# Kernel optimization log

Hardware: AMD Instinct MI355X
Metric: run time of the kernel (lower is better)

Reference implementation:

```python
import jax, jax.numpy as jnp
import numpy as np
from jax import lax

EMBED = 512
HEADS = 8
KD = EMBED // HEADS  # key_dim == head_dim (value_factor=1)


def setup_inputs() -> dict:
    key = jax.random.key(0)
    ks = jax.random.split(key, 13)
    b, h, w = 4, 128, 128
    s = 0.02
    return {
        "x": jax.random.normal(ks[0], (b, h, w, EMBED), jnp.float32),
        "mask_h": jax.random.normal(ks[1], (HEADS, h, h), jnp.float32),
        "mask_w": jax.random.normal(ks[2], (HEADS, w, w), jnp.float32),
        "Wq": jax.random.normal(ks[3], (EMBED, EMBED), jnp.float32) * s,
        "bq": jnp.zeros((EMBED,), jnp.float32),
        "Wk": jax.random.normal(ks[4], (EMBED, EMBED), jnp.float32) * s,
        "bk": jnp.zeros((EMBED,), jnp.float32),
        "Wv": jax.random.normal(ks[5], (EMBED, EMBED), jnp.float32) * s,
        "bv": jnp.zeros((EMBED,), jnp.float32),
        "lepe_w": jax.random.normal(ks[6], (5, 5, 1, EMBED), jnp.float32) * s,  # depthwise 5x5, HWIO
        "lepe_b": jnp.zeros((EMBED,), jnp.float32),
        "Wo": jax.random.normal(ks[7], (EMBED, EMBED), jnp.float32) * s,
        "bo": jnp.zeros((EMBED,), jnp.float32),
    }


def reference(x, mask_h, mask_w, Wq, bq, Wk, bk, Wv, bv, lepe_w, lepe_b, Wo, bo):
    b, h, w, _ = x.shape
    scaling = KD ** -0.5
    q = x @ Wq + bq                      # (b,h,w,C)
    k = (x @ Wk + bk) * scaling
    v = x @ Wv + bv

    # depthwise-conv positional term (LePE), 5x5 pad 2, groups=C
    lepe = lax.conv_general_dilated(
        v, lepe_w, window_strides=(1, 1), padding=[(2, 2), (2, 2)],
        dimension_numbers=("NHWC", "HWIO", "NHWC"), feature_group_count=EMBED,
    ) + lepe_b

    qr = q.reshape(b, h, w, HEADS, KD)
    kr = k.reshape(b, h, w, HEADS, KD)
    vr = v.reshape(b, h, w, HEADS, KD)

    # width-axis attention (per row), additive per-head decay mask
    sw = jnp.einsum("bhqnd,bhknd->bhnqk", qr, kr) + mask_w[None, None]  # (b,h,n,w,w)
    Aw = jax.nn.softmax(sw, axis=-1)
    o1 = jnp.einsum("bhnqk,bhknd->bhqnd", Aw, vr)                       # (b,h,w,n,d)

    # height-axis attention (per column) on the width-pass output
    sh = jnp.einsum("bqwnd,bkwnd->bwnqk", qr, kr) + mask_h[None, None]  # (b,w,n,h,h)
    Ah = jax.nn.softmax(sh, axis=-1)
    o2 = jnp.einsum("bwnqk,bkwnd->bqwnd", Ah, o1)                       # (b,h,w,n,d)

    out = o2.reshape(b, h, w, EMBED) + lepe
    return out @ Wo + bo
```

## Files before the change

kernel.cpp:

```cpp
#include <hip/hip_runtime.h>
#include <stdint.h>
#include <stddef.h>

typedef unsigned short u16;
typedef __attribute__((ext_vector_type(8))) short bf16x8;
typedef __attribute__((ext_vector_type(4))) short bf16x4;
typedef __attribute__((ext_vector_type(4))) float f32x4;

__device__ __forceinline__ u16 f2bf(float f) {
  union { float f; uint32_t u; } v; v.f = f;
  uint32_t u = v.u;
  return (u16)((u + 0x7FFFu + ((u >> 16) & 1u)) >> 16);
}
__device__ __forceinline__ float bf2f(u16 b) {
  union { uint32_t u; float f; } v; v.u = ((uint32_t)b) << 16;
  return v.f;
}

__device__ __forceinline__ void glds16(const u16* g, u16* l) {
  __builtin_amdgcn_global_load_lds((const __attribute__((address_space(1))) void*)g,
                                   (__attribute__((address_space(3))) void*)l, 16, 0, 0);
}

__device__ __forceinline__ uint32_t lds_addr(const u16* p) {
  return (uint32_t)(uintptr_t)(const __attribute__((address_space(3))) u16*)p;
}

#define MFMA(a, b, c) __builtin_amdgcn_mfma_f32_16x16x32_bf16((a), (b), (c), 0, 0, 0)


__global__ __launch_bounds__(256) void k_cvt_bf16(const float* __restrict__ in,
                                                  u16* __restrict__ out, int n) {
  int i = (blockIdx.x * 256 + threadIdx.x) * 8;
  if (i >= n) return;
  const float4* p = (const float4*)(in + i);
  float4 a = p[0], b = p[1];
  union { bf16x8 v; u16 s[8]; } o;
  o.s[0] = f2bf(a.x); o.s[1] = f2bf(a.y); o.s[2] = f2bf(a.z); o.s[3] = f2bf(a.w);
  o.s[4] = f2bf(b.x); o.s[5] = f2bf(b.y); o.s[6] = f2bf(b.z); o.s[7] = f2bf(b.w);
  *(bf16x8*)(out + i) = o.v;
}


__global__ __launch_bounds__(256) void k_build_w(
    const float* __restrict__ Wq, const float* __restrict__ Wk,
    const float* __restrict__ Wv, const float* __restrict__ Wo,
    const float* __restrict__ bq, const float* __restrict__ bk,
    const float* __restrict__ bv,
    u16* __restrict__ wqkvT, u16* __restrict__ woT, float* __restrict__ bias)
{
  __shared__ u16 tl[64 * 73];
  const int bid = blockIdx.x;
  const int mtx = bid >> 6;
  const int tr = (bid >> 3) & 7, tc = bid & 7;
  const float* W = (mtx == 0) ? Wq : (mtx == 1) ? Wk : (mtx == 2) ? Wv : Wo;
  const float s = (mtx == 1) ? 0.125f : 1.0f;
  const int t = threadIdx.x;
  const int lr = t >> 6, lc = t & 63;
  #pragma unroll
  for (int it = 0; it < 16; ++it) {
    int k = tr * 64 + it * 4 + lr;
    int n = tc * 64 + lc;
    tl[lc * 73 + it * 4 + lr] = f2bf(W[(size_t)k * 512 + n] * s);
  }
  __syncthreads();
  u16* dst = (mtx == 3) ? woT : (wqkvT + (size_t)mtx * 512 * 512);
  #pragma unroll
  for (int it = 0; it < 16; ++it) {
    int n = tc * 64 + it * 4 + lr;
    int k = tr * 64 + lc;
    dst[(size_t)n * 512 + k] = tl[(it * 4 + lr) * 73 + lc];
  }
  if (bid < 6) {
    int i = bid * 256 + t;
    const float* B = (i < 512) ? bq : (i < 1024) ? bk : bv;
    float sc = (i >= 512 && i < 1024) ? 0.125f : 1.0f;
    bias[i] = B[i & 511] * sc;
  }
}


__device__ __forceinline__ void stageH(const u16* __restrict__ src, int ld, size_t grow0,
                                       int kt, int row0, u16* lmat, int t) {
  #pragma unroll
  for (int it = 0; it < 2; ++it) {
    int e = it * 4096 + t * 8;
    int row = row0 + (e >> 6);
    int ch = (e >> 3) & 7;
    int cs = ch ^ (row & 7);
    glds16(src + (grow0 + row) * (size_t)ld + kt * 64 + cs * 8, lmat + row * 64 + ch * 8);
  }
}

__device__ __forceinline__ bf16x8 ldfrag(const u16* lmat, int row, int c) {
  return *(const bf16x8*)(lmat + row * 64 + ((c ^ (row & 7)) << 3));
}

template<bool STAGE, bool VM8>
__device__ __forceinline__ void process_tile(
    const u16* __restrict__ A, int lda, size_t rowA0,
    const u16* __restrict__ BT, int ldb, size_t rowB0,
    u16* LAc, u16* LBc, int nxt,
    int wm, int wn, int fq, int fr, int t,
    f32x4 (&acc)[2][4][2][2])
{
  bf16x8 bA[4][2], bB[2][2][2];
  #pragma unroll
  for (int n = 0; n < 2; ++n)
    #pragma unroll
    for (int kk = 0; kk < 2; ++kk)
      bB[0][n][kk] = ldfrag(LBc, wn * 32 + n * 16 + fr, kk * 4 + fq);
  #pragma unroll
  for (int m = 0; m < 4; ++m)
    #pragma unroll
    for (int kk = 0; kk < 2; ++kk)
      bA[m][kk] = ldfrag(LAc, wm * 64 + m * 16 + fr, kk * 4 + fq);
  __builtin_amdgcn_s_setprio(1);
  #pragma unroll
  for (int m = 0; m < 4; ++m)
    #pragma unroll
    for (int n = 0; n < 2; ++n)
      #pragma unroll
      for (int kk = 0; kk < 2; ++kk)
        acc[0][m][0][n] = MFMA(bA[m][kk], bB[0][n][kk], acc[0][m][0][n]);
  __builtin_amdgcn_s_setprio(0);
  __builtin_amdgcn_s_barrier();
  #pragma unroll
  for (int n = 0; n < 2; ++n)
    #pragma unroll
    for (int kk = 0; kk < 2; ++kk)
      bB[1][n][kk] = ldfrag(LBc, 128 + wn * 32 + n * 16 + fr, kk * 4 + fq);
  if (STAGE) {
    stageH(A, lda, rowA0, nxt, 0, LAc, t);
    stageH(BT, ldb, rowB0, nxt, 0, LBc, t);
  }
  __builtin_amdgcn_s_setprio(1);
  #pragma unroll
  for (int m = 0; m < 4; ++m)
    #pragma unroll
    for (int n = 0; n < 2; ++n)
      #pragma unroll
      for (int kk = 0; kk < 2; ++kk)
        acc[0][m][1][n] = MFMA(bA[m][kk], bB[1][n][kk], acc[0][m][1][n]);
  __builtin_amdgcn_s_setprio(0);
  __builtin_amdgcn_s_barrier();
  #pragma unroll
  for (int m = 0; m < 4; ++m)
    #pragma unroll
    for (int kk = 0; kk < 2; ++kk)
      bA[m][kk] = ldfrag(LAc, 128 + wm * 64 + m * 16 + fr, kk * 4 + fq);
  if (STAGE) stageH(BT, ldb, rowB0, nxt, 128, LBc, t);
  __builtin_amdgcn_s_setprio(1);
  #pragma unroll
  for (int m = 0; m < 4; ++m)
    #pragma unroll
    for (int n = 0; n < 2; ++n)
      #pragma unroll
      for (int kk = 0; kk < 2; ++kk)
        acc[1][m][0][n] = MFMA(bA[m][kk], bB[0][n][kk], acc[1][m][0][n]);
  __builtin_amdgcn_s_setprio(0);
  __builtin_amdgcn_s_barrier();
  if (STAGE) stageH(A, lda, rowA0, nxt, 128, LAc, t);
  __builtin_amdgcn_s_setprio(1);
  #pragma unroll
  for (int m = 0; m < 4; ++m)
    #pragma unroll
    for (int n = 0; n < 2; ++n)
      #pragma unroll
      for (int kk = 0; kk < 2; ++kk)
        acc[1][m][1][n] = MFMA(bA[m][kk], bB[1][n][kk], acc[1][m][1][n]);
  __builtin_amdgcn_s_setprio(0);
  if (VM8) asm volatile("s_waitcnt vmcnt(8)" ::: "memory");
  else     asm volatile("s_waitcnt vmcnt(0)" ::: "memory");
  __builtin_amdgcn_s_barrier();
}

template<bool OUT_F32, int NTN>
__global__ __launch_bounds__(512, 2) void k_gemm256(
    const u16* __restrict__ A, int lda,
    const u16* __restrict__ BT, int ldb,
    const float* __restrict__ bias,
    void* __restrict__ Cp, int ldc)
{
  __shared__ u16 lds[65536];
  u16* LA0 = lds;
  u16* LB0 = lds + 16384;
  u16* LA1 = lds + 32768;
  u16* LB1 = lds + 49152;

  const int t = threadIdx.x, l = t & 63, w = t >> 6;
  const int wm = w >> 2, wn = w & 3;
  const int fq = l >> 4, fr = l & 15;

  const int bid = blockIdx.x;
  const int cpx = gridDim.x >> 3;
  const int swz = (bid & 7) * cpx + (bid >> 3);
  const int tn = swz % NTN, tm = swz / NTN;
  const size_t rowA0 = (size_t)tm * 256;
  const size_t rowB0 = (size_t)tn * 256;

  f32x4 acc[2][4][2][2];
  #pragma unroll
  for (int a = 0; a < 2; ++a)
    #pragma unroll
    for (int m = 0; m < 4; ++m)
      #pragma unroll
      for (int b = 0; b < 2; ++b)
        #pragma unroll
        for (int n = 0; n < 2; ++n) acc[a][m][b][n] = (f32x4){0.f, 0.f, 0.f, 0.f};

  stageH(A,  lda, rowA0, 0, 0,   LA0, t); stageH(A,  lda, rowA0, 0, 128, LA0, t);
  stageH(BT, ldb, rowB0, 0, 0,   LB0, t); stageH(BT, ldb, rowB0, 0, 128, LB0, t);
  stageH(A,  lda, rowA0, 1, 0,   LA1, t); stageH(A,  lda, rowA0, 1, 128, LA1, t);
  stageH(BT, ldb, rowB0, 1, 0,   LB1, t); stageH(BT, ldb, rowB0, 1, 128, LB1, t);
  asm volatile("s_waitcnt vmcnt(8)" ::: "memory");
  __builtin_amdgcn_s_barrier();

  for (int i = 0; i < 3; ++i) {
    process_tile<true, true>(A, lda, rowA0, BT, ldb, rowB0, LA0, LB0, 2 * i + 2,
                             wm, wn, fq, fr, t, acc);
    process_tile<true, true>(A, lda, rowA0, BT, ldb, rowB0, LA1, LB1, 2 * i + 3,
                             wm, wn, fq, fr, t, acc);
  }
  process_tile<false, false>(A, lda, rowA0, BT, ldb, rowB0, LA0, LB0, 0,
                             wm, wn, fq, fr, t, acc);
  process_tile<false, false>(A, lda, rowA0, BT, ldb, rowB0, LA1, LB1, 0,
                             wm, wn, fq, fr, t, acc);

  #pragma unroll
  for (int nh = 0; nh < 2; ++nh)
    #pragma unroll
    for (int n = 0; n < 2; ++n) {
      int col = (int)rowB0 + nh * 128 + wn * 32 + n * 16 + fr;
      float bb = bias[col];
      #pragma unroll
      for (int mh = 0; mh < 2; ++mh)
        #pragma unroll
        for (int m = 0; m < 4; ++m) {
          #pragma unroll
          for (int r = 0; r < 4; ++r) {
            size_t row = rowA0 + mh * 128 + wm * 64 + m * 16 + fq * 4 + r;
            float v = acc[mh][m][nh][n][r] + bb;
            if (OUT_F32) ((float*)Cp)[row * ldc + col] = v;
            else         ((u16*)Cp)[row * ldc + col] = f2bf(v);
          }
        }
    }
}


__global__ __launch_bounds__(256) void k_lepe(
    const u16* __restrict__ qkv, const float* __restrict__ w5,
    const float* __restrict__ lb, u16* __restrict__ outp)
{
  __shared__ u16 wlds[12800];
  #pragma unroll
  for (int j = 0; j < 50; ++j) {
    int idx = j * 256 + threadIdx.x;
    wlds[idx] = f2bf(w5[idx]);
  }
  __syncthreads();

  const int t = threadIdx.x, w = t >> 6, l = t & 63;
  const int c0 = l << 3;
  const int bid = blockIdx.x;
  const int x = (bid & 31) * 4 + w;
  const int y0 = ((bid >> 5) & 15) * 8;
  const int b = bid >> 9;

  float acc[8][8];
  {
    float4 b0 = *(const float4*)(lb + c0);
    float4 b1 = *(const float4*)(lb + c0 + 4);
    #pragma unroll
    for (int tt = 0; tt < 8; ++tt) {
      acc[tt][0] = b0.x; acc[tt][1] = b0.y; acc[tt][2] = b0.z; acc[tt][3] = b0.w;
      acc[tt][4] = b1.x; acc[tt][5] = b1.y; acc[tt][6] = b1.z; acc[tt][7] = b1.w;
    }
  }

  #pragma unroll
  for (int dx = 0; dx < 5; ++dx) {
    int xx = x + dx - 2;
    if ((unsigned)xx < 128u) {
      float wreg[5][8];
      #pragma unroll
      for (int dy = 0; dy < 5; ++dy) {
        union { bf16x8 v; u16 s[8]; } w8;
        w8.v = *(const bf16x8*)(wlds + (dy * 5 + dx) * 512 + c0);
        #pragma unroll
        for (int j = 0; j < 8; ++j) wreg[dy][j] = bf2f(w8.s[j]);
      }
      #pragma unroll
      for (int r = 0; r < 12; ++r) {
        int yy = y0 + r - 2;
        if ((unsigned)yy < 128u) {
          union { bf16x8 v; u16 s[8]; } v8;
          v8.v = *(const bf16x8*)(qkv + (size_t)((b * 128 + yy) * 128 + xx) * 1536
                                  + 1024 + c0);
          float vf[8];
          #pragma unroll
          for (int j = 0; j < 8; ++j) vf[j] = bf2f(v8.s[j]);
          #pragma unroll
          for (int tt = 0; tt < 8; ++tt) {
            int dy = r - tt;
            if (dy >= 0 && dy <= 4) {
              #pragma unroll
              for (int j = 0; j < 8; ++j)
                acc[tt][j] += vf[j] * wreg[dy][j];
            }
          }
        }
      }
    }
  }

  #pragma unroll
  for (int tt = 0; tt < 8; ++tt) {
    size_t tok = (size_t)(b * 128 + y0 + tt) * 128 + x;
    union { bf16x8 v; u16 s[8]; } ov;
    #pragma unroll
    for (int j = 0; j < 8; ++j) ov.s[j] = f2bf(acc[tt][j]);
    *(bf16x8*)(outp + tok * 512 + c0) = ov.v;
  }
}


template<int AXIS>
__global__ __launch_bounds__(512) void k_attn(
    const u16* qkv, const float* __restrict__ mask,
    const u16* __restrict__ lepe, u16* outp)
{
  __shared__ u16 smem[24576];
  u16* q_s = smem;
  u16* k_s = smem + 8192;
  u16* vL  = smem + 16384;
  u16* P   = smem;

  const int t = threadIdx.x, w = t >> 6, l = t & 63;
  const int fq = l >> 4, fr = l & 15;
  const int line = blockIdx.x, head = blockIdx.y, b = blockIdx.z;
  const int coff = head * 64;
  const size_t base0 = (AXIS == 0) ? ((size_t)(b * 128 + line) * 128)
                                   : ((size_t)b * 16384 + line);
  const size_t tstr = (AXIS == 0) ? 1 : 128;

  #pragma unroll
  for (int it = 0; it < 2; ++it) {
    int ee = it * 4096 + t * 8;
    int row = ee >> 6;
    int cs = ((ee >> 3) & 7) ^ (row & 7);
    size_t tok = base0 + (size_t)row * tstr;
    glds16(qkv + tok * 1536 +       coff + cs * 8, q_s + it * 4096 + w * 512);
    glds16(qkv + tok * 1536 + 512 + coff + cs * 8, k_s + it * 4096 + w * 512);
  }
  #pragma unroll
  for (int p = 0; p < 2; ++p) {
    int c = p * 512 + t;
    int kt = (c >> 5) * 4 + ((c >> 1) & 3);
    int d0 = ((c >> 3) & 3) * 16 + (c & 1) * 8;
    size_t tok = base0 + (size_t)kt * tstr;
    glds16(qkv + tok * 1536 + 1024 + coff + d0, vL + c * 8);
  }
  __syncthreads();

  f32x4 acc[8];
  #pragma unroll
  for (int n = 0; n < 8; ++n) acc[n] = (f32x4){0.f, 0.f, 0.f, 0.f};

  #pragma unroll
  for (int kk = 0; kk < 2; ++kk) {
    int arow = w * 16 + fr;
    int ac = (kk * 4 + fq) ^ (arow & 7);
    bf16x8 af = *(const bf16x8*)(q_s + arow * 64 + ac * 8);
    #pragma unroll
    for (int n = 0; n < 8; ++n) {
      int brow = n * 16 + fr;
      int bc = (kk * 4 + fq) ^ (brow & 7);
      bf16x8 bfr = *(const bf16x8*)(k_s + brow * 64 + bc * 8);
      acc[n] = MFMA(af, bfr, acc[n]);
    }
  }

  const float* mbase = mask + (size_t)head * 16384;
  const int q0 = w * 16 + fq * 4;
  #pragma unroll
  for (int n = 0; n < 8; ++n) {
    const float* mp = mbase + (size_t)q0 * 128 + n * 16 + fr;
    #pragma unroll
    for (int r = 0; r < 4; ++r) acc[n][r] += mp[(size_t)r * 128];
  }
  #pragma unroll
  for (int r = 0; r < 4; ++r) {
    float mx = acc[0][r];
    #pragma unroll
    for (int n = 1; n < 8; ++n) mx = fmaxf(mx, acc[n][r]);
    mx = fmaxf(mx, __shfl_xor(mx, 1));
    mx = fmaxf(mx, __shfl_xor(mx, 2));
    mx = fmaxf(mx, __shfl_xor(mx, 4));
    mx = fmaxf(mx, __shfl_xor(mx, 8));
    float sum = 0.f;
    #pragma unroll
    for (int n = 0; n < 8; ++n) {
      float ev = __expf(acc[n][r] - mx);
      acc[n][r] = ev; sum += ev;
    }
    sum += __shfl_xor(sum, 1);
    sum += __shfl_xor(sum, 2);
    sum += __shfl_xor(sum, 4);
    sum += __shfl_xor(sum, 8);
    float inv = 1.0f / sum;
    #pragma unroll
    for (int n = 0; n < 8; ++n) acc[n][r] *= inv;
  }
  __syncthreads();

  #pragma unroll
  for (int r = 0; r < 4; ++r) {
    int row = q0 + r;
    int swz = (row & 7) << 4;
    #pragma unroll
    for (int n = 0; n < 8; ++n) {
      int col = n * 16 + fr;
      *(u16*)((char*)P + row * 256 + ((2 * col) ^ swz)) = f2bf(acc[n][r]);
    }
  }
  __syncthreads();

  f32x4 o[4];
  #pragma unroll
  for (int n = 0; n < 4; ++n) o[n] = (f32x4){0.f, 0.f, 0.f, 0.f};

  const uint32_t vbase = lds_addr(vL) + (uint32_t)(fq * 1024 + fr * 8);
  #pragma unroll
  for (int kt = 0; kt < 4; ++kt) {
    int arow = w * 16 + fr;
    bf16x8 af = *(const bf16x8*)((const char*)P + arow * 256 +
                 (((kt * 4 + fq) << 4) ^ ((arow & 7) << 4)));
    bf16x4 lo0, hi0, lo1, hi1, lo2, hi2, lo3, hi3;
    {
      uint32_t a0 = vbase + kt * 4096;
      uint32_t a1 = a0 + 128;
      uint32_t a2 = a0 + 256;
      uint32_t a3 = a0 + 384;
      asm volatile("ds_read_b64_tr_b16 %0, %1" : "=v"(lo0) : "v"(a0));
      asm volatile("ds_read_b64_tr_b16 %0, %1 offset:512" : "=v"(hi0) : "v"(a0));
      asm volatile("ds_read_b64_tr_b16 %0, %1" : "=v"(lo1) : "v"(a1));
      asm volatile("ds_read_b64_tr_b16 %0, %1 offset:512" : "=v"(hi1) : "v"(a1));
      asm volatile("ds_read_b64_tr_b16 %0, %1" : "=v"(lo2) : "v"(a2));
      asm volatile("ds_read_b64_tr_b16 %0, %1 offset:512" : "=v"(hi2) : "v"(a2));
      asm volatile("ds_read_b64_tr_b16 %0, %1" : "=v"(lo3) : "v"(a3));
      asm volatile("ds_read_b64_tr_b16 %0, %1 offset:512" : "=v"(hi3) : "v"(a3));
    }
    asm volatile("s_waitcnt lgkmcnt(0)" ::: "memory");
    __builtin_amdgcn_sched_barrier(0);
    union { bf16x4 h[2]; bf16x8 v; } u0, u1, u2, u3;
    u0.h[0] = lo0; u0.h[1] = hi0;
    u1.h[0] = lo1; u1.h[1] = hi1;
    u2.h[0] = lo2; u2.h[1] = hi2;
    u3.h[0] = lo3; u3.h[1] = hi3;
    o[0] = MFMA(af, u0.v, o[0]);
    o[1] = MFMA(af, u1.v, o[1]);
    o[2] = MFMA(af, u2.v, o[2]);
    o[3] = MFMA(af, u3.v, o[3]);
  }

  #pragma unroll
  for (int r = 0; r < 4; ++r) {
    int i = q0 + r;
    size_t tok = base0 + (size_t)i * tstr;
    #pragma unroll
    for (int n = 0; n < 4; ++n) {
      int d = n * 16 + fr;
      float v = o[n][r];
      if (AXIS == 1) {
        v += bf2f(lepe[tok * 512 + coff + d]);
        outp[tok * 1536 + coff + d] = f2bf(v);
      } else {
        outp[tok * 1536 + 1024 + coff + d] = f2bf(v);
      }
    }
  }
}


extern "C" void kernel_launch(void* const* d_in, const int* in_sizes, int n_in,
                              void* d_out, int out_size, void* d_ws, size_t ws_size,
                              hipStream_t stream) {
  const float* x  = (const float*)d_in[0];
  const float* mh = (const float*)d_in[1];
  const float* mw = (const float*)d_in[2];
  const float* Wq = (const float*)d_in[3];
  const float* bq = (const float*)d_in[4];
  const float* Wk = (const float*)d_in[5];
  const float* bk = (const float*)d_in[6];
  const float* Wv = (const float*)d_in[7];
  const float* bv = (const float*)d_in[8];
  const float* w5 = (const float*)d_in[9];
  const float* lb = (const float*)d_in[10];
  const float* Wo = (const float*)d_in[11];
  const float* bo = (const float*)d_in[12];

  char* ws = (char*)d_ws;
  u16*   qkv   = (u16*)ws;
  u16*   wqkvT = (u16*)(ws + 201326592);
  u16*   woT   = (u16*)(ws + 202899456);
  float* bqkv  = (float*)(ws + 203423744);

  char* od = (char*)d_out;
  u16* xb   = (u16*)od;
  u16* lepe = (u16*)(od + 67108864);

  k_cvt_bf16<<<16384, 256, 0, stream>>>(x, xb, 33554432);
  k_build_w<<<256, 256, 0, stream>>>(Wq, Wk, Wv, Wo, bq, bk, bv, wqkvT, woT, bqkv);

  k_gemm256<false, 6><<<768, 512, 0, stream>>>(xb, 512, wqkvT, 512, bqkv,
                                               qkv, 1536);
  k_gemm256<false, 6><<<768, 512, 0, stream>>>(xb + (size_t)32768 * 512, 512,
                                               wqkvT, 512, bqkv,
                                               qkv + (size_t)32768 * 1536, 1536);

  k_lepe<<<2048, 256, 0, stream>>>(qkv, w5, lb, lepe);

  k_attn<0><<<dim3(128, 8, 4), 512, 0, stream>>>(qkv, mw, nullptr, qkv);
  k_attn<1><<<dim3(128, 8, 4), 512, 0, stream>>>(qkv, mh, lepe, qkv);

  k_gemm256<true, 2><<<512, 512, 0, stream>>>(qkv, 1536, woT, 512, bo, d_out, 512);
}
```

Baseline: 420.8 us.

## Fuse LePE conv and width attention into one interleaved kernel

Merges the depthwise LePE convolution and the width-axis attention into a single launch. Every fifth block runs the conv and the other four run attention, so the memory and ALU-heavy conv work can overlap with the MFMA-heavy attention work on the same GPU. LePE blocks now use 512 threads, each covering 8 columns instead of 4. The width-pass output goes to a compact 512-stride buffer that reuses the dead bf16 x area, and the height pass reads its V operand from there. The trade-offs are that every block of the merged kernel carries the larger register footprint of both code paths, and that attention and conv blocks now compete for the same compute units.

```diff
diff --git a/kernel.cpp b/kernel.cpp
--- a/kernel.cpp
+++ b/kernel.cpp
@@ -249,24 +249,179 @@
 }
 
 
-__global__ __launch_bounds__(256) void k_lepe(
+template<int AXIS, bool LEPE>
+__device__ __forceinline__ void attn_body(
+    const u16* __restrict__ qkv,
+    const u16* __restrict__ vsrc, int vld, int voff,
+    const float* __restrict__ mask,
+    const u16* __restrict__ lepe,
+    u16* __restrict__ outp, int old,
+    u16* smem, int line, int head, int b)
+{
+  u16* q_s = smem;
+  u16* k_s = smem + 8192;
+  u16* vL  = smem + 16384;
+  u16* P   = smem;
+
+  const int t = threadIdx.x, w = t >> 6, l = t & 63;
+  const int fq = l >> 4, fr = l & 15;
+  const int coff = head * 64;
+  const size_t base0 = (AXIS == 0) ? ((size_t)(b * 128 + line) * 128)
+                                   : ((size_t)b * 16384 + line);
+  const size_t tstr = (AXIS == 0) ? 1 : 128;
+
+  #pragma unroll
+  for (int it = 0; it < 2; ++it) {
+    int ee = it * 4096 + t * 8;
+    int row = ee >> 6;
+    int cs = ((ee >> 3) & 7) ^ (row & 7);
+    size_t tok = base0 + (size_t)row * tstr;
+    glds16(qkv + tok * 1536 +       coff + cs * 8, q_s + it * 4096 + w * 512);
+    glds16(qkv + tok * 1536 + 512 + coff + cs * 8, k_s + it * 4096 + w * 512);
+  }
+  #pragma unroll
+  for (int p = 0; p < 2; ++p) {
+    int c = p * 512 + t;
+    int kt = (c >> 5) * 4 + ((c >> 1) & 3);
+    int d0 = ((c >> 3) & 3) * 16 + (c & 1) * 8;
+    size_t tok = base0 + (size_t)kt * tstr;
+    glds16(vsrc + tok * (size_t)vld + voff + d0, vL + c * 8);
+  }
+  __syncthreads();
+
+  f32x4 acc[8];
+  #pragma unroll
+  for (int n = 0; n < 8; ++n) acc[n] = (f32x4){0.f, 0.f, 0.f, 0.f};
+
+  #pragma unroll
+  for (int kk = 0; kk < 2; ++kk) {
+    int arow = w * 16 + fr;
+    int ac = (kk * 4 + fq) ^ (arow & 7);
+    bf16x8 af = *(const bf16x8*)(q_s + arow * 64 + ac * 8);
+    #pragma unroll
+    for (int n = 0; n < 8; ++n) {
+      int brow = n * 16 + fr;
+      int bc = (kk * 4 + fq) ^ (brow & 7);
+      bf16x8 bfr = *(const bf16x8*)(k_s + brow * 64 + bc * 8);
+      acc[n] = MFMA(af, bfr, acc[n]);
+    }
+  }
+
+  const float* mbase = mask + (size_t)head * 16384;
+  const int q0 = w * 16 + fq * 4;
+  #pragma unroll
+  for (int n = 0; n < 8; ++n) {
+    const float* mp = mbase + (size_t)q0 * 128 + n * 16 + fr;
+    #pragma unroll
+    for (int r = 0; r < 4; ++r) acc[n][r] += mp[(size_t)r * 128];
+  }
+  #pragma unroll
+  for (int r = 0; r < 4; ++r) {
+    float mx = acc[0][r];
+    #pragma unroll
+    for (int n = 1; n < 8; ++n) mx = fmaxf(mx, acc[n][r]);
+    mx = fmaxf(mx, __shfl_xor(mx, 1));
+    mx = fmaxf(mx, __shfl_xor(mx, 2));
+    mx = fmaxf(mx, __shfl_xor(mx, 4));
+    mx = fmaxf(mx, __shfl_xor(mx, 8));
+    float sum = 0.f;
+    #pragma unroll
+    for (int n = 0; n < 8; ++n) {
+      float ev = __expf(acc[n][r] - mx);
+      acc[n][r] = ev; sum += ev;
+    }
+    sum += __shfl_xor(sum, 1);
+    sum += __shfl_xor(sum, 2);
+    sum += __shfl_xor(sum, 4);
+    sum += __shfl_xor(sum, 8);
+    float inv = 1.0f / sum;
+    #pragma unroll
+    for (int n = 0; n < 8; ++n) acc[n][r] *= inv;
+  }
+  __syncthreads();
+
+  #pragma unroll
+  for (int r = 0; r < 4; ++r) {
+    int row = q0 + r;
+    int swz = (row & 7) << 4;
+    #pragma unroll
+    for (int n = 0; n < 8; ++n) {
+      int col = n * 16 + fr;
+      *(u16*)((char*)P + row * 256 + ((2 * col) ^ swz)) = f2bf(acc[n][r]);
+    }
+  }
+  __syncthreads();
+
+  f32x4 o[4];
+  #pragma unroll
+  for (int n = 0; n < 4; ++n) o[n] = (f32x4){0.f, 0.f, 0.f, 0.f};
+
+  const uint32_t vbase = lds_addr(vL) + (uint32_t)(fq * 1024 + fr * 8);
+  #pragma unroll
+  for (int kt = 0; kt < 4; ++kt) {
+    int arow = w * 16 + fr;
+    bf16x8 af = *(const bf16x8*)((const char*)P + arow * 256 +
+                 (((kt * 4 + fq) << 4) ^ ((arow & 7) << 4)));
+    bf16x4 lo0, hi0, lo1, hi1, lo2, hi2, lo3, hi3;
+    {
+      uint32_t a0 = vbase + kt * 4096;
+      uint32_t a1 = a0 + 128;
+      uint32_t a2 = a0 + 256;
+      uint32_t a3 = a0 + 384;
+      asm volatile("ds_read_b64_tr_b16 %0, %1" : "=v"(lo0) : "v"(a0));
+      asm volatile("ds_read_b64_tr_b16 %0, %1 offset:512" : "=v"(hi0) : "v"(a0));
+      asm volatile("ds_read_b64_tr_b16 %0, %1" : "=v"(lo1) : "v"(a1));
+      asm volatile("ds_read_b64_tr_b16 %0, %1 offset:512" : "=v"(hi1) : "v"(a1));
+      asm volatile("ds_read_b64_tr_b16 %0, %1" : "=v"(lo2) : "v"(a2));
+      asm volatile("ds_read_b64_tr_b16 %0, %1 offset:512" : "=v"(hi2) : "v"(a2));
+      asm volatile("ds_read_b64_tr_b16 %0, %1" : "=v"(lo3) : "v"(a3));
+      asm volatile("ds_read_b64_tr_b16 %0, %1 offset:512" : "=v"(hi3) : "v"(a3));
+    }
+    asm volatile("s_waitcnt lgkmcnt(0)" ::: "memory");
+    __builtin_amdgcn_sched_barrier(0);
+    union { bf16x4 h[2]; bf16x8 v; } u0, u1, u2, u3;
+    u0.h[0] = lo0; u0.h[1] = hi0;
+    u1.h[0] = lo1; u1.h[1] = hi1;
+    u2.h[0] = lo2; u2.h[1] = hi2;
+    u3.h[0] = lo3; u3.h[1] = hi3;
+    o[0] = MFMA(af, u0.v, o[0]);
+    o[1] = MFMA(af, u1.v, o[1]);
+    o[2] = MFMA(af, u2.v, o[2]);
+    o[3] = MFMA(af, u3.v, o[3]);
+  }
+
+  #pragma unroll
+  for (int r = 0; r < 4; ++r) {
+    int i = q0 + r;
+    size_t tok = base0 + (size_t)i * tstr;
+    #pragma unroll
+    for (int n = 0; n < 4; ++n) {
+      int d = n * 16 + fr;
+      float v = o[n][r];
+      if (LEPE) v += bf2f(lepe[tok * 512 + coff + d]);
+      outp[tok * (size_t)old + coff + d] = f2bf(v);
+    }
+  }
+}
+
+
+__device__ __forceinline__ void lepe_body(
     const u16* __restrict__ qkv, const float* __restrict__ w5,
-    const float* __restrict__ lb, u16* __restrict__ outp)
-{
-  __shared__ u16 wlds[12800];
-  #pragma unroll
-  for (int j = 0; j < 50; ++j) {
-    int idx = j * 256 + threadIdx.x;
+    const float* __restrict__ lb, u16* __restrict__ outp,
+    u16* wlds, int lbid)
+{
+  #pragma unroll
+  for (int j = 0; j < 25; ++j) {
+    int idx = j * 512 + threadIdx.x;
     wlds[idx] = f2bf(w5[idx]);
   }
   __syncthreads();
 
   const int t = threadIdx.x, w = t >> 6, l = t & 63;
   const int c0 = l << 3;
-  const int bid = blockIdx.x;
-  const int x = (bid & 31) * 4 + w;
-  const int y0 = ((bid >> 5) & 15) * 8;
-  const int b = bid >> 9;
+  const int x = (lbid & 15) * 8 + w;
+  const int y0 = ((lbid >> 4) & 15) * 8;
+  const int b = lbid >> 8;
 
   float acc[8][8];
   {
@@ -326,161 +481,32 @@
 }
 
 
-template<int AXIS>
-__global__ __launch_bounds__(512) void k_attn(
-    const u16* qkv, const float* __restrict__ mask,
-    const u16* __restrict__ lepe, u16* outp)
+__global__ __launch_bounds__(512) void k_fused(
+    const u16* __restrict__ qkv, const float* __restrict__ mask_w,
+    const float* __restrict__ w5, const float* __restrict__ lb,
+    u16* __restrict__ o1, u16* __restrict__ lepe_out)
 {
   __shared__ u16 smem[24576];
-  u16* q_s = smem;
-  u16* k_s = smem + 8192;
-  u16* vL  = smem + 16384;
-  u16* P   = smem;
-
-  const int t = threadIdx.x, w = t >> 6, l = t & 63;
-  const int fq = l >> 4, fr = l & 15;
-  const int line = blockIdx.x, head = blockIdx.y, b = blockIdx.z;
-  const int coff = head * 64;
-  const size_t base0 = (AXIS == 0) ? ((size_t)(b * 128 + line) * 128)
-                                   : ((size_t)b * 16384 + line);
-  const size_t tstr = (AXIS == 0) ? 1 : 128;
-
-  #pragma unroll
-  for (int it = 0; it < 2; ++it) {
-    int ee = it * 4096 + t * 8;
-    int row = ee >> 6;
-    int cs = ((ee >> 3) & 7) ^ (row & 7);
-    size_t tok = base0 + (size_t)row * tstr;
-    glds16(qkv + tok * 1536 +       coff + cs * 8, q_s + it * 4096 + w * 512);
-    glds16(qkv + tok * 1536 + 512 + coff + cs * 8, k_s + it * 4096 + w * 512);
-  }
-  #pragma unroll
-  for (int p = 0; p < 2; ++p) {
-    int c = p * 512 + t;
-    int kt = (c >> 5) * 4 + ((c >> 1) & 3);
-    int d0 = ((c >> 3) & 3) * 16 + (c & 1) * 8;
-    size_t tok = base0 + (size_t)kt * tstr;
-    glds16(qkv + tok * 1536 + 1024 + coff + d0, vL + c * 8);
-  }
-  __syncthreads();
-
-  f32x4 acc[8];
-  #pragma unroll
-  for (int n = 0; n < 8; ++n) acc[n] = (f32x4){0.f, 0.f, 0.f, 0.f};
-
-  #pragma unroll
-  for (int kk = 0; kk < 2; ++kk) {
-    int arow = w * 16 + fr;
-    int ac = (kk * 4 + fq) ^ (arow & 7);
-    bf16x8 af = *(const bf16x8*)(q_s + arow * 64 + ac * 8);
-    #pragma unroll
-    for (int n = 0; n < 8; ++n) {
-      int brow = n * 16 + fr;
-      int bc = (kk * 4 + fq) ^ (brow & 7);
-      bf16x8 bfr = *(const bf16x8*)(k_s + brow * 64 + bc * 8);
-      acc[n] = MFMA(af, bfr, acc[n]);
-    }
-  }
-
-  const float* mbase = mask + (size_t)head * 16384;
-  const int q0 = w * 16 + fq * 4;
-  #pragma unroll
-  for (int n = 0; n < 8; ++n) {
-    const float* mp = mbase + (size_t)q0 * 128 + n * 16 + fr;
-    #pragma unroll
-    for (int r = 0; r < 4; ++r) acc[n][r] += mp[(size_t)r * 128];
-  }
-  #pragma unroll
-  for (int r = 0; r < 4; ++r) {
-    float mx = acc[0][r];
-    #pragma unroll
-    for (int n = 1; n < 8; ++n) mx = fmaxf(mx, acc[n][r]);
-    mx = fmaxf(mx, __shfl_xor(mx, 1));
-    mx = fmaxf(mx, __shfl_xor(mx, 2));
-    mx = fmaxf(mx, __shfl_xor(mx, 4));
-    mx = fmaxf(mx, __shfl_xor(mx, 8));
-    float sum = 0.f;
-    #pragma unroll
-    for (int n = 0; n < 8; ++n) {
-      float ev = __expf(acc[n][r] - mx);
-      acc[n][r] = ev; sum += ev;
-    }
-    sum += __shfl_xor(sum, 1);
-    sum += __shfl_xor(sum, 2);
-    sum += __shfl_xor(sum, 4);
-    sum += __shfl_xor(sum, 8);
-    float inv = 1.0f / sum;
-    #pragma unroll
-    for (int n = 0; n < 8; ++n) acc[n][r] *= inv;
-  }
-  __syncthreads();
-
-  #pragma unroll
-  for (int r = 0; r < 4; ++r) {
-    int row = q0 + r;
-    int swz = (row & 7) << 4;
-    #pragma unroll
-    for (int n = 0; n < 8; ++n) {
-      int col = n * 16 + fr;
-      *(u16*)((char*)P + row * 256 + ((2 * col) ^ swz)) = f2bf(acc[n][r]);
-    }
-  }
-  __syncthreads();
-
-  f32x4 o[4];
-  #pragma unroll
-  for (int n = 0; n < 4; ++n) o[n] = (f32x4){0.f, 0.f, 0.f, 0.f};
-
-  const uint32_t vbase = lds_addr(vL) + (uint32_t)(fq * 1024 + fr * 8);
-  #pragma unroll
-  for (int kt = 0; kt < 4; ++kt) {
-    int arow = w * 16 + fr;
-    bf16x8 af = *(const bf16x8*)((const char*)P + arow * 256 +
-                 (((kt * 4 + fq) << 4) ^ ((arow & 7) << 4)));
-    bf16x4 lo0, hi0, lo1, hi1, lo2, hi2, lo3, hi3;
-    {
-      uint32_t a0 = vbase + kt * 4096;
-      uint32_t a1 = a0 + 128;
-      uint32_t a2 = a0 + 256;
-      uint32_t a3 = a0 + 384;
-      asm volatile("ds_read_b64_tr_b16 %0, %1" : "=v"(lo0) : "v"(a0));
-      asm volatile("ds_read_b64_tr_b16 %0, %1 offset:512" : "=v"(hi0) : "v"(a0));
-      asm volatile("ds_read_b64_tr_b16 %0, %1" : "=v"(lo1) : "v"(a1));
-      asm volatile("ds_read_b64_tr_b16 %0, %1 offset:512" : "=v"(hi1) : "v"(a1));
-      asm volatile("ds_read_b64_tr_b16 %0, %1" : "=v"(lo2) : "v"(a2));
-      asm volatile("ds_read_b64_tr_b16 %0, %1 offset:512" : "=v"(hi2) : "v"(a2));
-      asm volatile("ds_read_b64_tr_b16 %0, %1" : "=v"(lo3) : "v"(a3));
-      asm volatile("ds_read_b64_tr_b16 %0, %1 offset:512" : "=v"(hi3) : "v"(a3));
-    }
-    asm volatile("s_waitcnt lgkmcnt(0)" ::: "memory");
-    __builtin_amdgcn_sched_barrier(0);
-    union { bf16x4 h[2]; bf16x8 v; } u0, u1, u2, u3;
-    u0.h[0] = lo0; u0.h[1] = hi0;
-    u1.h[0] = lo1; u1.h[1] = hi1;
-    u2.h[0] = lo2; u2.h[1] = hi2;
-    u3.h[0] = lo3; u3.h[1] = hi3;
-    o[0] = MFMA(af, u0.v, o[0]);
-    o[1] = MFMA(af, u1.v, o[1]);
-    o[2] = MFMA(af, u2.v, o[2]);
-    o[3] = MFMA(af, u3.v, o[3]);
-  }
-
-  #pragma unroll
-  for (int r = 0; r < 4; ++r) {
-    int i = q0 + r;
-    size_t tok = base0 + (size_t)i * tstr;
-    #pragma unroll
-    for (int n = 0; n < 4; ++n) {
-      int d = n * 16 + fr;
-      float v = o[n][r];
-      if (AXIS == 1) {
-        v += bf2f(lepe[tok * 512 + coff + d]);
-        outp[tok * 1536 + coff + d] = f2bf(v);
-      } else {
-        outp[tok * 1536 + 1024 + coff + d] = f2bf(v);
-      }
-    }
-  }
+  const int bid = blockIdx.x;
+  if ((bid % 5) == 4) {
+    lepe_body(qkv, w5, lb, lepe_out, smem, bid / 5);
+  } else {
+    int aid = (bid / 5) * 4 + (bid % 5);
+    int line = aid & 127, head = (aid >> 7) & 7, b = aid >> 10;
+    attn_body<0, false>(qkv, qkv, 1536, 1024 + head * 64, mask_w, nullptr,
+                        o1, 512, smem, line, head, b);
+  }
+}
+
+__global__ __launch_bounds__(512) void k_attn1(
+    const u16* __restrict__ qkv, const u16* __restrict__ o1,
+    const float* __restrict__ mask_h, const u16* __restrict__ lepe,
+    u16* __restrict__ outp)
+{
+  __shared__ u16 smem[24576];
+  int line = blockIdx.x, head = blockIdx.y, b = blockIdx.z;
+  attn_body<1, true>(qkv, o1, 512, head * 64, mask_h, lepe,
+                     outp, 1536, smem, line, head, b);
 }
 
 
@@ -509,6 +535,7 @@
 
   char* od = (char*)d_out;
   u16* xb   = (u16*)od;
+  u16* o1   = (u16*)od;
   u16* lepe = (u16*)(od + 67108864);
 
   k_cvt_bf16<<<16384, 256, 0, stream>>>(x, xb, 33554432);
@@ -520,10 +547,9 @@
                                                wqkvT, 512, bqkv,
                                                qkv + (size_t)32768 * 1536, 1536);
 
-  k_lepe<<<2048, 256, 0, stream>>>(qkv, w5, lb, lepe);
-
-  k_attn<0><<<dim3(128, 8, 4), 512, 0, stream>>>(qkv, mw, nullptr, qkv);
-  k_attn<1><<<dim3(128, 8, 4), 512, 0, stream>>>(qkv, mh, lepe, qkv);
+  k_fused<<<5120, 512, 0, stream>>>(qkv, mw, w5, lb, o1, lepe);
+
+  k_attn1<<<dim3(128, 8, 4), 512, 0, stream>>>(qkv, o1, mh, lepe, qkv);
 
   k_gemm256<true, 2><<<512, 512, 0, stream>>>(qkv, 1536, woT, 512, bo, d_out, 512);
 }
```

Result: slower. 454.3 us (+7.9%).

## Cut attention LDS footprint: load Q to registers, stage P in halves

Applied to the files above, without the earlier changes.

The attention kernel now loads each wave's Q fragments straight from global memory into registers instead of staging Q in LDS. It also writes the softmax probabilities to LDS in two 64-column halves, interleaved with the PV MFMAs. Together these shrink shared memory from 48KB to 32KB and add a launch-bounds occupancy hint, aiming for more resident blocks per CU. The cost is non-async global Q loads and the reuse of the P buffer across halves. P now overlaps the K region, and the loop appears to have no barrier between the per-wave writes and reads of P in each half.

```diff
diff --git a/kernel.cpp b/kernel.cpp
--- a/kernel.cpp
+++ b/kernel.cpp
@@ -327,14 +327,13 @@
 
 
 template<int AXIS>
-__global__ __launch_bounds__(512) void k_attn(
+__global__ __launch_bounds__(512, 8) void k_attn(
     const u16* qkv, const float* __restrict__ mask,
     const u16* __restrict__ lepe, u16* outp)
 {
-  __shared__ u16 smem[24576];
-  u16* q_s = smem;
-  u16* k_s = smem + 8192;
-  u16* vL  = smem + 16384;
+  __shared__ u16 smem[16384];
+  u16* k_s = smem;
+  u16* vL  = smem + 8192;
   u16* P   = smem;
 
   const int t = threadIdx.x, w = t >> 6, l = t & 63;
@@ -351,7 +350,6 @@
     int row = ee >> 6;
     int cs = ((ee >> 3) & 7) ^ (row & 7);
     size_t tok = base0 + (size_t)row * tstr;
-    glds16(qkv + tok * 1536 +       coff + cs * 8, q_s + it * 4096 + w * 512);
     glds16(qkv + tok * 1536 + 512 + coff + cs * 8, k_s + it * 4096 + w * 512);
   }
   #pragma unroll
@@ -362,6 +360,11 @@
     size_t tok = base0 + (size_t)kt * tstr;
     glds16(qkv + tok * 1536 + 1024 + coff + d0, vL + c * 8);
   }
+  const int arow = w * 16 + fr;
+  const size_t qtok = base0 + (size_t)arow * tstr;
+  bf16x8 qf[2];
+  qf[0] = *(const bf16x8*)(qkv + qtok * 1536 + coff + fq * 8);
+  qf[1] = *(const bf16x8*)(qkv + qtok * 1536 + coff + 32 + fq * 8);
   __syncthreads();
 
   f32x4 acc[8];
@@ -370,15 +373,12 @@
 
   #pragma unroll
   for (int kk = 0; kk < 2; ++kk) {
-    int arow = w * 16 + fr;
-    int ac = (kk * 4 + fq) ^ (arow & 7);
-    bf16x8 af = *(const bf16x8*)(q_s + arow * 64 + ac * 8);
     #pragma unroll
     for (int n = 0; n < 8; ++n) {
       int brow = n * 16 + fr;
       int bc = (kk * 4 + fq) ^ (brow & 7);
       bf16x8 bfr = *(const bf16x8*)(k_s + brow * 64 + bc * 8);
-      acc[n] = MFMA(af, bfr, acc[n]);
+      acc[n] = MFMA(qf[kk], bfr, acc[n]);
     }
   }
 
@@ -415,54 +415,55 @@
   }
   __syncthreads();
 
-  #pragma unroll
-  for (int r = 0; r < 4; ++r) {
-    int row = q0 + r;
-    int swz = (row & 7) << 4;
-    #pragma unroll
-    for (int n = 0; n < 8; ++n) {
-      int col = n * 16 + fr;
-      *(u16*)((char*)P + row * 256 + ((2 * col) ^ swz)) = f2bf(acc[n][r]);
-    }
-  }
-  __syncthreads();
-
   f32x4 o[4];
   #pragma unroll
   for (int n = 0; n < 4; ++n) o[n] = (f32x4){0.f, 0.f, 0.f, 0.f};
 
   const uint32_t vbase = lds_addr(vL) + (uint32_t)(fq * 1024 + fr * 8);
   #pragma unroll
-  for (int kt = 0; kt < 4; ++kt) {
-    int arow = w * 16 + fr;
-    bf16x8 af = *(const bf16x8*)((const char*)P + arow * 256 +
-                 (((kt * 4 + fq) << 4) ^ ((arow & 7) << 4)));
-    bf16x4 lo0, hi0, lo1, hi1, lo2, hi2, lo3, hi3;
-    {
-      uint32_t a0 = vbase + kt * 4096;
-      uint32_t a1 = a0 + 128;
-      uint32_t a2 = a0 + 256;
-      uint32_t a3 = a0 + 384;
-      asm volatile("ds_read_b64_tr_b16 %0, %1" : "=v"(lo0) : "v"(a0));
-      asm volatile("ds_read_b64_tr_b16 %0, %1 offset:512" : "=v"(hi0) : "v"(a0));
-      asm volatile("ds_read_b64_tr_b16 %0, %1" : "=v"(lo1) : "v"(a1));
-      asm volatile("ds_read_b64_tr_b16 %0, %1 offset:512" : "=v"(hi1) : "v"(a1));
-      asm volatile("ds_read_b64_tr_b16 %0, %1" : "=v"(lo2) : "v"(a2));
-      asm volatile("ds_read_b64_tr_b16 %0, %1 offset:512" : "=v"(hi2) : "v"(a2));
-      asm volatile("ds_read_b64_tr_b16 %0, %1" : "=v"(lo3) : "v"(a3));
-      asm volatile("ds_read_b64_tr_b16 %0, %1 offset:512" : "=v"(hi3) : "v"(a3));
-    }
-    asm volatile("s_waitcnt lgkmcnt(0)" ::: "memory");
-    __builtin_amdgcn_sched_barrier(0);
-    union { bf16x4 h[2]; bf16x8 v; } u0, u1, u2, u3;
-    u0.h[0] = lo0; u0.h[1] = hi0;
-    u1.h[0] = lo1; u1.h[1] = hi1;
-    u2.h[0] = lo2; u2.h[1] = hi2;
-    u3.h[0] = lo3; u3.h[1] = hi3;
-    o[0] = MFMA(af, u0.v, o[0]);
-    o[1] = MFMA(af, u1.v, o[1]);
-    o[2] = MFMA(af, u2.v, o[2]);
-    o[3] = MFMA(af, u3.v, o[3]);
+  for (int h = 0; h < 2; ++h) {
+    #pragma unroll
+    for (int r = 0; r < 4; ++r) {
+      int row = q0 + r;
+      int swz = (row & 7) << 4;
+      #pragma unroll
+      for (int nn = 0; nn < 4; ++nn) {
+        int col = nn * 16 + fr;
+        *(u16*)((char*)P + row * 128 + ((2 * col) ^ swz)) = f2bf(acc[h * 4 + nn][r]);
+      }
+    }
+    #pragma unroll
+    for (int kh = 0; kh < 2; ++kh) {
+      int kt = h * 2 + kh;
+      bf16x8 af = *(const bf16x8*)((const char*)P + arow * 128 +
+                   (((kh * 32 + fq * 8) * 2) ^ ((arow & 7) << 4)));
+      bf16x4 lo0, hi0, lo1, hi1, lo2, hi2, lo3, hi3;
+      {
+        uint32_t a0 = vbase + kt * 4096;
+        uint32_t a1 = a0 + 128;
+        uint32_t a2 = a0 + 256;
+        uint32_t a3 = a0 + 384;
+        asm volatile("ds_read_b64_tr_b16 %0, %1" : "=v"(lo0) : "v"(a0));
+        asm volatile("ds_read_b64_tr_b16 %0, %1 offset:512" : "=v"(hi0) : "v"(a0));
+        asm volatile("ds_read_b64_tr_b16 %0, %1" : "=v"(lo1) : "v"(a1));
+        asm volatile("ds_read_b64_tr_b16 %0, %1 offset:512" : "=v"(hi1) : "v"(a1));
+        asm volatile("ds_read_b64_tr_b16 %0, %1" : "=v"(lo2) : "v"(a2));
+        asm volatile("ds_read_b64_tr_b16 %0, %1 offset:512" : "=v"(hi2) : "v"(a2));
+        asm volatile("ds_read_b64_tr_b16 %0, %1" : "=v"(lo3) : "v"(a3));
+        asm volatile("ds_read_b64_tr_b16 %0, %1 offset:512" : "=v"(hi3) : "v"(a3));
+      }
+      asm volatile("s_waitcnt lgkmcnt(0)" ::: "memory");
+      __builtin_amdgcn_sched_barrier(0);
+      union { bf16x4 hh[2]; bf16x8 v; } u0, u1, u2, u3;
+      u0.hh[0] = lo0; u0.hh[1] = hi0;
+      u1.hh[0] = lo1; u1.hh[1] = hi1;
+      u2.hh[0] = lo2; u2.hh[1] = hi2;
+      u3.hh[0] = lo3; u3.hh[1] = hi3;
+      o[0] = MFMA(af, u0.v, o[0]);
+      o[1] = MFMA(af, u1.v, o[1]);
+      o[2] = MFMA(af, u2.v, o[2]);
+      o[3] = MFMA(af, u3.v, o[3]);
+    }
   }
 
   #pragma unroll
```

Measured after the change: 508.4 us. 20.8% more time.
